# Optimization experiments

Measured on AMD Instinct MI355X. Metric: run time of the kernel, lower is better.

## Reference

```python
import jax, jax.numpy as jnp
from jax import lax
import numpy as np

# Guide bandwidths (sigma^2) for the cross-bilateral weights.
SIGMA_ALBEDO = 0.01
SIGMA_NORMAL = 0.1
SIGMA_DEPTH = 0.1
EPS = 1e-10

B, H, W = 4, 720, 1280
WIN = 11


def setup_inputs() -> dict:
    key = jax.random.key(0)
    k1, k2, k3, k4 = jax.random.split(key, 4)
    inp = jax.random.normal(k1, (B, 3, H, W), dtype=jnp.float32)
    albedo = jax.random.uniform(k2, (B, 3, H, W), dtype=jnp.float32)
    normal = jax.random.normal(k3, (B, 3, H, W), dtype=jnp.float32)
    normal = normal / (jnp.linalg.norm(normal, axis=1, keepdims=True) + EPS)
    depth = jax.random.uniform(k4, (B, 1, H, W), dtype=jnp.float32)
    return {"input": inp, "albedo": albedo, "normal": normal,
            "depth": depth, "win_size": WIN}


def _cross_bilateral(inp, albedo, normal, depth, win_size):
    pad = win_size // 2
    b, c, h, w = inp.shape

    def pad4(x):
        return jnp.pad(x, ((0, 0), (0, 0), (pad, pad), (pad, pad)), mode="edge")

    ip, ap, np_, dp = pad4(inp), pad4(albedo), pad4(normal), pad4(depth)

    # All (dy, dx) taps in the window, scanned to keep memory O(B*C*H*W).
    offs = jnp.asarray([(dy, dx) for dy in range(win_size) for dx in range(win_size)],
                       dtype=jnp.int32)

    def tap(carry, off):
        acc, wsum = carry
        dy, dx = off[0], off[1]

        def sl(x):
            return lax.dynamic_slice(x, (0, 0, dy, dx), (b, x.shape[1], h, w))

        dA = jnp.sum((albedo - sl(ap)) ** 2, axis=1, keepdims=True)  # [B,1,H,W]
        dN = jnp.sum((normal - sl(np_)) ** 2, axis=1, keepdims=True)
        dD = (depth - sl(dp)) ** 2
        wgt = jnp.exp(-(dA / SIGMA_ALBEDO + dN / SIGMA_NORMAL + dD / SIGMA_DEPTH))
        return (acc + wgt * sl(ip), wsum + wgt), None

    init = (jnp.zeros_like(inp), jnp.zeros((b, 1, h, w), dtype=inp.dtype))
    (acc, wsum), _ = lax.scan(tap, init, offs)
    return acc / jnp.maximum(wsum, EPS)


def reference(input, albedo, normal, depth, win_size):
    return _cross_bilateral(input, albedo, normal, depth, win_size)
```

## Files before the change

kernel.cpp:

```cpp
#include <hip/hip_runtime.h>
#include <math.h>


#define HH   720
#define WW   1280
#define PAD  5
#define WIN  11
#define TW   32
#define TH   32
#define HW2  42

typedef _Float16 h2 __attribute__((ext_vector_type(2)));

__device__ __forceinline__ unsigned pk2(float a, float b) {
    unsigned lo = __builtin_bit_cast(unsigned short, (_Float16)a);
    unsigned hi = __builtin_bit_cast(unsigned short, (_Float16)b);
    return lo | (hi << 16);
}

__device__ __forceinline__ float fdot2(h2 a, h2 b, float c) {
#if __has_builtin(__builtin_amdgcn_fdot2)
    return __builtin_amdgcn_fdot2(a, b, c, false);
#else
    return fmaf((float)a.x, (float)b.x, fmaf((float)a.y, (float)b.y, c));
#endif
}

__device__ __forceinline__ h2 bch2(unsigned u) { return __builtin_bit_cast(h2, u); }

struct Ctr { h2 c0, c1, c2, c3; };

__device__ __forceinline__ void tap_one(const Ctr& c, uint4 g, h2 i01, h2 i2s,
                                        float4& a) {
    h2 d0 = bch2(g.x) - c.c0;
    h2 d1 = bch2(g.y) - c.c1;
    h2 d2 = bch2(g.z) - c.c2;
    h2 d3 = bch2(g.w) - c.c3;
    float e = fdot2(d0, d0, fdot2(d1, d1, fdot2(d2, d2, fdot2(d3, d3, 0.f))));
    float w = __builtin_amdgcn_exp2f(-e);
    a.x = fmaf(w, (float)i01.x, a.x);
    a.y = fmaf(w, (float)i01.y, a.y);
    a.z = fmaf(w, (float)i2s.x, a.z);
    a.w += w;
}

template<int KLO, int KHI>
__device__ __forceinline__ void do_row(const uint4* __restrict__ rg,
                                       const uint2* __restrict__ ri,
                                       const Ctr* c, float4* acc) {
#pragma unroll
    for (int dx = 0; dx < WIN; ++dx) {
        uint4 g  = rg[dx];
        uint2 t  = ri[dx];
        h2 i01 = bch2(t.x), i2s = bch2(t.y);
#pragma unroll
        for (int k = KLO; k <= KHI; ++k)
            tap_one(c[k], g, i01, i2s, acc[k]);
    }
}

__global__ __launch_bounds__(256, 3)
void xbilateral_kernel(const float* __restrict__ inp,
                       const float* __restrict__ alb,
                       const float* __restrict__ nrm,
                       const float* __restrict__ dep,
                       float* __restrict__ out)
{
    __shared__ uint4 sG[HW2][HW2];
    __shared__ uint2 sI[HW2][HW2];

    const int tid = threadIdx.x;
    const int lx  = tid & 31;
    const int ly  = tid >> 5;
    const int bx0 = blockIdx.x * TW;
    const int by0 = blockIdx.y * TH;
    const int b   = blockIdx.z;

    const float kA = 12.01122406f;
    const float kN = 3.79828255f;

    const size_t plane = (size_t)HH * WW;
    const float* albB = alb + (size_t)b * 3 * plane;
    const float* nrmB = nrm + (size_t)b * 3 * plane;
    const float* inpB = inp + (size_t)b * 3 * plane;
    const float* depB = dep + (size_t)b * plane;

    for (int idx = tid; idx < HW2 * HW2; idx += 256) {
        int r = idx / HW2;
        int c = idx - r * HW2;
        int gy = by0 + r - PAD; gy = min(max(gy, 0), HH - 1);
        int gx = bx0 + c - PAD; gx = min(max(gx, 0), WW - 1);
        size_t o = (size_t)gy * WW + gx;
        float a0 = albB[o] * kA, a1 = albB[plane + o] * kA, a2 = albB[2 * plane + o] * kA;
        float n0 = nrmB[o] * kN, n1 = nrmB[plane + o] * kN, n2 = nrmB[2 * plane + o] * kN;
        float d0 = depB[o] * kN;
        sG[r][c] = make_uint4(pk2(a0, a1), pk2(a2, d0), pk2(n0, n1), pk2(n2, 0.f));
        float i0 = inpB[o], i1 = inpB[plane + o], i2 = inpB[2 * plane + o];
        sI[r][c] = make_uint2(pk2(i0, i1), pk2(i2, 1.f));
    }
    __syncthreads();

    const int py0 = 4 * ly;

    Ctr c[4];
#pragma unroll
    for (int k = 0; k < 4; ++k) {
        uint4 g = sG[py0 + k + PAD][lx + PAD];
        c[k].c0 = bch2(g.x);
        c[k].c1 = bch2(g.y);
        c[k].c2 = bch2(g.z);
        c[k].c3 = bch2(g.w);
    }

    float4 acc[4];
#pragma unroll
    for (int k = 0; k < 4; ++k) acc[k] = make_float4(0.f, 0.f, 0.f, 0.f);

    do_row<0, 0>(&sG[py0 + 0][lx], &sI[py0 + 0][lx], c, acc);
    do_row<0, 1>(&sG[py0 + 1][lx], &sI[py0 + 1][lx], c, acc);
    do_row<0, 2>(&sG[py0 + 2][lx], &sI[py0 + 2][lx], c, acc);
#pragma unroll 1
    for (int t = 3; t <= 10; ++t)
        do_row<0, 3>(&sG[py0 + t][lx], &sI[py0 + t][lx], c, acc);
    do_row<1, 3>(&sG[py0 + 11][lx], &sI[py0 + 11][lx], c, acc);
    do_row<2, 3>(&sG[py0 + 12][lx], &sI[py0 + 12][lx], c, acc);
    do_row<3, 3>(&sG[py0 + 13][lx], &sI[py0 + 13][lx], c, acc);

    const int ox = bx0 + lx;
    float* outB = out + (size_t)b * 3 * plane;
#pragma unroll
    for (int k = 0; k < 4; ++k) {
        int oy = by0 + py0 + k;
        if (oy < HH) {
            float inv = 1.0f / fmaxf(acc[k].w, 1e-10f);
            size_t o = (size_t)oy * WW + ox;
            outB[o]             = acc[k].x * inv;
            outB[plane + o]     = acc[k].y * inv;
            outB[2 * plane + o] = acc[k].z * inv;
        }
    }
}

extern "C" void kernel_launch(void* const* d_in, const int* in_sizes, int n_in,
                              void* d_out, int out_size, void* d_ws, size_t ws_size,
                              hipStream_t stream) {
    const float* inp = (const float*)d_in[0];
    const float* alb = (const float*)d_in[1];
    const float* nrm = (const float*)d_in[2];
    const float* dep = (const float*)d_in[3];
    float* out = (float*)d_out;

    dim3 grid(WW / TW, (HH + TH - 1) / TH, 4);
    dim3 block(256);
    xbilateral_kernel<<<grid, block, 0, stream>>>(inp, alb, nrm, dep, out);
}
```

Baseline: 248.6 us.

## Expand squared guide distance into dot products with precomputed norms in fp32

Replaces the packed-fp16 difference-and-dot2 weight computation with an algebraic expansion, ||g||^2/2 + ||c||^2/2 - g·c, using fp32 guide values plus a per-pixel precomputed half-norm stored in shared memory. Row boundaries are now handled by a uniform 14-row loop that masks out-of-window center rows with a large negative bias instead of using specialized row templates. Shared memory grows (two float4 planes) and occupancy hint drops from 3 to 2 blocks, while the inner loop is not unrolled and uses software prefetch. This trades fp16 packed math for fp32 FMAs and raises LDS traffic, with possible cancellation error from the expanded form.

```diff
diff --git a/kernel.cpp b/kernel.cpp
--- a/kernel.cpp
+++ b/kernel.cpp
@@ -17,57 +17,18 @@
     unsigned hi = __builtin_bit_cast(unsigned short, (_Float16)b);
     return lo | (hi << 16);
 }
-
-__device__ __forceinline__ float fdot2(h2 a, h2 b, float c) {
-#if __has_builtin(__builtin_amdgcn_fdot2)
-    return __builtin_amdgcn_fdot2(a, b, c, false);
-#else
-    return fmaf((float)a.x, (float)b.x, fmaf((float)a.y, (float)b.y, c));
-#endif
-}
-
 __device__ __forceinline__ h2 bch2(unsigned u) { return __builtin_bit_cast(h2, u); }
 
-struct Ctr { h2 c0, c1, c2, c3; };
-
-__device__ __forceinline__ void tap_one(const Ctr& c, uint4 g, h2 i01, h2 i2s,
-                                        float4& a) {
-    h2 d0 = bch2(g.x) - c.c0;
-    h2 d1 = bch2(g.y) - c.c1;
-    h2 d2 = bch2(g.z) - c.c2;
-    h2 d3 = bch2(g.w) - c.c3;
-    float e = fdot2(d0, d0, fdot2(d1, d1, fdot2(d2, d2, fdot2(d3, d3, 0.f))));
-    float w = __builtin_amdgcn_exp2f(-e);
-    a.x = fmaf(w, (float)i01.x, a.x);
-    a.y = fmaf(w, (float)i01.y, a.y);
-    a.z = fmaf(w, (float)i2s.x, a.z);
-    a.w += w;
-}
-
-template<int KLO, int KHI>
-__device__ __forceinline__ void do_row(const uint4* __restrict__ rg,
-                                       const uint2* __restrict__ ri,
-                                       const Ctr* c, float4* acc) {
-#pragma unroll
-    for (int dx = 0; dx < WIN; ++dx) {
-        uint4 g  = rg[dx];
-        uint2 t  = ri[dx];
-        h2 i01 = bch2(t.x), i2s = bch2(t.y);
-#pragma unroll
-        for (int k = KLO; k <= KHI; ++k)
-            tap_one(c[k], g, i01, i2s, acc[k]);
-    }
-}
-
-__global__ __launch_bounds__(256, 3)
+__global__ __launch_bounds__(256, 2)
 void xbilateral_kernel(const float* __restrict__ inp,
                        const float* __restrict__ alb,
                        const float* __restrict__ nrm,
                        const float* __restrict__ dep,
                        float* __restrict__ out)
 {
-    __shared__ uint4 sG[HW2][HW2];
-    __shared__ uint2 sI[HW2][HW2];
+    __shared__ float4 sGA[HW2][HW2];
+    __shared__ float4 sGB[HW2][HW2];
+    __shared__ uint2  sI [HW2][HW2];
 
     const int tid = threadIdx.x;
     const int lx  = tid & 31;
@@ -76,8 +37,8 @@
     const int by0 = blockIdx.y * TH;
     const int b   = blockIdx.z;
 
-    const float kA = 12.01122406f;
-    const float kN = 3.79828255f;
+    const float kA2 = 16.98653137f;
+    const float kN2 = 5.37154913f;
 
     const size_t plane = (size_t)HH * WW;
     const float* albB = alb + (size_t)b * 3 * plane;
@@ -91,10 +52,13 @@
         int gy = by0 + r - PAD; gy = min(max(gy, 0), HH - 1);
         int gx = bx0 + c - PAD; gx = min(max(gx, 0), WW - 1);
         size_t o = (size_t)gy * WW + gx;
-        float a0 = albB[o] * kA, a1 = albB[plane + o] * kA, a2 = albB[2 * plane + o] * kA;
-        float n0 = nrmB[o] * kN, n1 = nrmB[plane + o] * kN, n2 = nrmB[2 * plane + o] * kN;
-        float d0 = depB[o] * kN;
-        sG[r][c] = make_uint4(pk2(a0, a1), pk2(a2, d0), pk2(n0, n1), pk2(n2, 0.f));
+        float a0 = albB[o] * kA2, a1 = albB[plane + o] * kA2, a2 = albB[2 * plane + o] * kA2;
+        float n0 = nrmB[o] * kN2, n1 = nrmB[plane + o] * kN2, n2 = nrmB[2 * plane + o] * kN2;
+        float d0 = depB[o] * kN2;
+        float gg = 0.5f * (a0 * a0 + a1 * a1 + a2 * a2 + d0 * d0 +
+                           n0 * n0 + n1 * n1 + n2 * n2);
+        sGA[r][c] = make_float4(a0, a1, a2, d0);
+        sGB[r][c] = make_float4(n0, n1, n2, gg);
         float i0 = inpB[o], i1 = inpB[plane + o], i2 = inpB[2 * plane + o];
         sI[r][c] = make_uint2(pk2(i0, i1), pk2(i2, 1.f));
     }
@@ -102,43 +66,76 @@
 
     const int py0 = 4 * ly;
 
-    Ctr c[4];
-#pragma unroll
-    for (int k = 0; k < 4; ++k) {
-        uint4 g = sG[py0 + k + PAD][lx + PAD];
-        c[k].c0 = bch2(g.x);
-        c[k].c1 = bch2(g.y);
-        c[k].c2 = bch2(g.z);
-        c[k].c3 = bch2(g.w);
+    float4 cA0 = sGA[py0 + 0 + PAD][lx + PAD], cB0 = sGB[py0 + 0 + PAD][lx + PAD];
+    float4 cA1 = sGA[py0 + 1 + PAD][lx + PAD], cB1 = sGB[py0 + 1 + PAD][lx + PAD];
+    float4 cA2 = sGA[py0 + 2 + PAD][lx + PAD], cB2 = sGB[py0 + 2 + PAD][lx + PAD];
+    float4 cA3 = sGA[py0 + 3 + PAD][lx + PAD], cB3 = sGB[py0 + 3 + PAD][lx + PAD];
+    float bn0 = -cB0.w, bn1 = -cB1.w, bn2 = -cB2.w, bn3 = -cB3.w;
+
+    float4 a0 = make_float4(0.f, 0.f, 0.f, 0.f);
+    float4 a1 = make_float4(0.f, 0.f, 0.f, 0.f);
+    float4 a2 = make_float4(0.f, 0.f, 0.f, 0.f);
+    float4 a3 = make_float4(0.f, 0.f, 0.f, 0.f);
+
+    const float KILL = -1e30f;
+
+#pragma unroll 1
+    for (int t = 0; t < 14; ++t) {
+        float bk0 = ((unsigned)(t - 0) <= 10u) ? bn0 : KILL;
+        float bk1 = ((unsigned)(t - 1) <= 10u) ? bn1 : KILL;
+        float bk2 = ((unsigned)(t - 2) <= 10u) ? bn2 : KILL;
+        float bk3 = ((unsigned)(t - 3) <= 10u) ? bn3 : KILL;
+
+        const float4* pA = &sGA[py0 + t][lx];
+        const float4* pB = &sGB[py0 + t][lx];
+        const uint2*  pI = &sI [py0 + t][lx];
+
+        float4 ga = pA[0], gb = pB[0];
+        uint2  ti = pI[0];
+
+#pragma unroll 1
+        for (int dx = 0; dx < WIN; ++dx) {
+            int nx = dx + 1; nx = (nx > WIN - 1) ? (WIN - 1) : nx;
+            float4 gan = pA[nx], gbn = pB[nx];
+            uint2  tin = pI[nx];
+
+            h2 lo = bch2(ti.x), hi = bch2(ti.y);
+            float i0 = (float)lo.x, i1 = (float)lo.y, i2 = (float)hi.x;
+            float ggt = gb.w;
+
+#define TAP(K)                                                                  \
+            {                                                                   \
+                float s = fmaf(ga.x, cA##K.x, fmaf(ga.y, cA##K.y,               \
+                          fmaf(ga.z, cA##K.z, fmaf(ga.w, cA##K.w,               \
+                          fmaf(gb.x, cB##K.x, fmaf(gb.y, cB##K.y,               \
+                          fmaf(gb.z, cB##K.z, bk##K - ggt)))))));               \
+                float w = __builtin_amdgcn_exp2f(s);                            \
+                a##K.x = fmaf(w, i0, a##K.x);                                   \
+                a##K.y = fmaf(w, i1, a##K.y);                                   \
+                a##K.z = fmaf(w, i2, a##K.z);                                   \
+                a##K.w += w;                                                    \
+            }
+            TAP(0) TAP(1) TAP(2) TAP(3)
+#undef TAP
+            ga = gan; gb = gbn; ti = tin;
+        }
     }
-
-    float4 acc[4];
-#pragma unroll
-    for (int k = 0; k < 4; ++k) acc[k] = make_float4(0.f, 0.f, 0.f, 0.f);
-
-    do_row<0, 0>(&sG[py0 + 0][lx], &sI[py0 + 0][lx], c, acc);
-    do_row<0, 1>(&sG[py0 + 1][lx], &sI[py0 + 1][lx], c, acc);
-    do_row<0, 2>(&sG[py0 + 2][lx], &sI[py0 + 2][lx], c, acc);
-#pragma unroll 1
-    for (int t = 3; t <= 10; ++t)
-        do_row<0, 3>(&sG[py0 + t][lx], &sI[py0 + t][lx], c, acc);
-    do_row<1, 3>(&sG[py0 + 11][lx], &sI[py0 + 11][lx], c, acc);
-    do_row<2, 3>(&sG[py0 + 12][lx], &sI[py0 + 12][lx], c, acc);
-    do_row<3, 3>(&sG[py0 + 13][lx], &sI[py0 + 13][lx], c, acc);
 
     const int ox = bx0 + lx;
     float* outB = out + (size_t)b * 3 * plane;
-#pragma unroll
-    for (int k = 0; k < 4; ++k) {
-        int oy = by0 + py0 + k;
-        if (oy < HH) {
-            float inv = 1.0f / fmaxf(acc[k].w, 1e-10f);
-            size_t o = (size_t)oy * WW + ox;
-            outB[o]             = acc[k].x * inv;
-            outB[plane + o]     = acc[k].y * inv;
-            outB[2 * plane + o] = acc[k].z * inv;
-        }
+#define WOUT(K)                                                                 \
+    {                                                                           \
+        int oy = by0 + py0 + K;                                                 \
+        if (oy < HH) {                                                          \
+            float inv = 1.0f / fmaxf(a##K.w, 1e-10f);                           \
+            size_t o = (size_t)oy * WW + ox;                                    \
+            outB[o]             = a##K.x * inv;                                 \
+            outB[plane + o]     = a##K.y * inv;                                 \
+            outB[2 * plane + o] = a##K.z * inv;                                 \
+        }                                                                       \
     }
+    WOUT(0) WOUT(1) WOUT(2) WOUT(3)
+#undef WOUT
 }
 
 extern "C" void kernel_launch(void* const* d_in, const int* in_sizes, int n_in,
```

Measured after the change: 296.5 us. 1.19x slower.
